# Optimization experiments

Hardware: AMD Instinct MI355X
Metric: run time of the kernel (lower is better)

Reference implementation:

```python
import jax, jax.numpy as jnp
import numpy as np

VOCAB, D_MODEL, N_EXPERTS, TOP_K = 32000, 768, 8, 2
D_FF = 4 * D_MODEL
BATCH, SEQ = 2, 2048


def setup_inputs() -> dict:
    key = jax.random.key(0)
    ks = jax.random.split(key, 6)
    s = 0.02
    return {
        "x": jax.random.randint(ks[0], (BATCH, SEQ), 0, VOCAB),
        "emb": jax.random.normal(ks[1], (VOCAB, D_MODEL), jnp.float32) * s,
        "gate_w": jax.random.normal(ks[2], (D_MODEL, N_EXPERTS), jnp.float32) * s,
        "gate_b": jnp.zeros((N_EXPERTS,), jnp.float32),
        "exp_w": jax.random.normal(ks[3], (N_EXPERTS, D_MODEL, D_FF), jnp.float32) * s,
        "exp_b": jnp.zeros((N_EXPERTS, D_FF), jnp.float32),
        "head_w": jax.random.normal(ks[4], (D_FF, VOCAB), jnp.float32) * s,
        "head_b": jnp.zeros((VOCAB,), jnp.float32),
    }


def reference(x, emb, gate_w, gate_b, exp_w, exp_b, head_w, head_b):
    B, S = x.shape
    h = emb[x]                                   # [B,S,D] embedding gather
    t = h.reshape(B * S, -1)                     # [T,D] token view
    logits = t @ gate_w + gate_b                 # [T,E] router
    topv, topi = jax.lax.top_k(logits, TOP_K)    # top-2 routing
    w = jax.nn.softmax(topv, axis=-1)            # renormalized gate weights
    T = t.shape[0]
    gates = jnp.zeros_like(logits).at[jnp.arange(T)[:, None], topi].set(w)  # [T,E]
    # expert FFN: Linear(d_model -> 4*d_model) + ReLU, dense over experts
    exp_out = jax.nn.relu(jnp.einsum('td,edf->tef', t, exp_w) + exp_b)      # [T,E,F]
    moe = jnp.einsum('te,tef->tf', gates, exp_out)                          # combine
    out = moe @ head_w + head_b                  # [T,V]
    return out.reshape(B, S, -1)
```

## Files before the change

kernel.cpp:

```cpp
#include <hip/hip_runtime.h>

typedef unsigned short u16;
typedef __attribute__((ext_vector_type(8))) short short8;
typedef __attribute__((ext_vector_type(4))) float f32x4;

#define T_TOKENS 4096
#define DMODEL   768
#define DFF      3072
#define NEXP     8
#define NVOCAB   32000

__device__ __forceinline__ u16 f2bf(float f) {
  unsigned u = __float_as_uint(f);
  u += 0x7FFFu + ((u >> 16) & 1u);
  return (u16)(u >> 16);
}

__device__ __forceinline__ void async_load16(const void* g, void* lds) {
  __builtin_amdgcn_global_load_lds((const __attribute__((address_space(1))) void*)g,
                                   (__attribute__((address_space(3))) void*)lds,
                                   16, 0, 0);
}

#define SBAR() __builtin_amdgcn_s_barrier()
#define VMCNT(n) asm volatile("s_waitcnt vmcnt(" #n ")")

__global__ __launch_bounds__(256) void k_embed_router(
    const int* __restrict__ x, const float* __restrict__ emb,
    const float* __restrict__ gw, const float* __restrict__ gb,
    u16* __restrict__ tbf, float* __restrict__ gates)
{
  __shared__ float partial[4][NEXP];
  const int t = blockIdx.x;
  const int tok = x[t];
  const float* er = emb + (size_t)tok * DMODEL;
  float p[NEXP];
#pragma unroll
  for (int e = 0; e < NEXP; ++e) p[e] = 0.f;
#pragma unroll
  for (int i = 0; i < 3; ++i) {
    const int d = threadIdx.x + i * 256;
    const float v = er[d];
    tbf[(size_t)t * DMODEL + d] = f2bf(v);
#pragma unroll
    for (int e = 0; e < NEXP; ++e) p[e] += v * gw[d * NEXP + e];
  }
#pragma unroll
  for (int e = 0; e < NEXP; ++e)
#pragma unroll
    for (int m = 32; m >= 1; m >>= 1) p[e] += __shfl_xor(p[e], m);
  const int lane = threadIdx.x & 63, wv = threadIdx.x >> 6;
  if (lane == 0)
    for (int e = 0; e < NEXP; ++e) partial[wv][e] = p[e];
  __syncthreads();
  if (threadIdx.x == 0) {
    float l[NEXP];
    for (int e = 0; e < NEXP; ++e)
      l[e] = partial[0][e] + partial[1][e] + partial[2][e] + partial[3][e] + gb[e];
    int i0 = 0;
    for (int e = 1; e < NEXP; ++e) if (l[e] > l[i0]) i0 = e;
    int i1 = -1;
    for (int e = 0; e < NEXP; ++e) { if (e == i0) continue; if (i1 < 0 || l[e] > l[i1]) i1 = e; }
    const float w0 = 1.f / (1.f + expf(l[i1] - l[i0]));
    float g[NEXP];
    for (int e = 0; e < NEXP; ++e) g[e] = 0.f;
    g[i0] = w0; g[i1] = 1.f - w0;
    for (int e = 0; e < NEXP; ++e) gates[t * NEXP + e] = g[e];
  }
}

__global__ __launch_bounds__(256) void k_transpose_cvt(
    const float* __restrict__ src, u16* __restrict__ dst, int R, int C)
{
  __shared__ float tile[32][33];
  const float* s = src + (size_t)blockIdx.z * R * C;
  u16* d = dst + (size_t)blockIdx.z * R * C;
  const int tx = threadIdx.x & 31, ty = threadIdx.x >> 5;
  const int c = blockIdx.x * 32 + tx;
#pragma unroll
  for (int i = 0; i < 4; ++i) {
    const int r = blockIdx.y * 32 + ty + i * 8;
    tile[ty + i * 8][tx] = s[(size_t)r * C + c];
  }
  __syncthreads();
  const int rr = blockIdx.y * 32 + tx;
#pragma unroll
  for (int i = 0; i < 4; ++i) {
    const int cc = blockIdx.x * 32 + ty + i * 8;
    d[(size_t)cc * R + rr] = f2bf(tile[tx][ty + i * 8]);
  }
}

__global__ __launch_bounds__(256) void k_ffn(
    const u16* __restrict__ A, const u16* __restrict__ BT,
    const float* __restrict__ gates, const float* __restrict__ eb,
    u16* __restrict__ moe)
{
  __shared__ u16 aT[128 * 64];
  __shared__ u16 bT[128 * 64];
  __shared__ float gLds[128][NEXP];
  const int tid = threadIdx.x;
  const int wave = tid >> 6, lane = tid & 63;
  const int wm = wave >> 1, wn = wave & 1;
  const int kg = lane >> 4, fr = lane & 15;
  const int m0 = blockIdx.y * 128, n0 = blockIdx.x * 128;

  for (int i = tid; i < 128 * NEXP; i += 256)
    gLds[i >> 3][i & 7] = gates[(size_t)(m0 + (i >> 3)) * NEXP + (i & 7)];

  f32x4 macc[4][4] = {};

  for (int e = 0; e < NEXP; ++e) {
    const u16* Be = BT + (size_t)e * DFF * DMODEL;
    f32x4 acc[4][4] = {};
    for (int ks = 0; ks < DMODEL / 64; ++ks) {
      __syncthreads();
      const int kb = ks * 64;
#pragma unroll
      for (int it = 0; it < 4; ++it) {
        const int c = it * 256 + tid;
        const int m = c >> 3;
        const int slot = (c & 7) ^ (m & 7);
        async_load16(A + (size_t)(m0 + m) * DMODEL + kb + slot * 8,
                     &aT[(it * 256 + wave * 64) * 8]);
        async_load16(Be + (size_t)(n0 + m) * DMODEL + kb + slot * 8,
                     &bT[(it * 256 + wave * 64) * 8]);
      }
      __syncthreads();
#pragma unroll
      for (int kk = 0; kk < 2; ++kk) {
        short8 af[4], bf[4];
#pragma unroll
        for (int i = 0; i < 4; ++i) {
          const int am = wm * 64 + i * 16 + fr;
          const int kc = kk * 4 + kg;
          af[i] = *(const short8*)&aT[(am * 8 + (kc ^ (am & 7))) * 8];
          const int bn = wn * 64 + i * 16 + fr;
          bf[i] = *(const short8*)&bT[(bn * 8 + (kc ^ (bn & 7))) * 8];
        }
#pragma unroll
        for (int i = 0; i < 4; ++i)
#pragma unroll
          for (int j = 0; j < 4; ++j)
            acc[i][j] = __builtin_amdgcn_mfma_f32_16x16x32_bf16(af[i], bf[j], acc[i][j], 0, 0, 0);
      }
    }
#pragma unroll
    for (int j = 0; j < 4; ++j) {
      const int col = n0 + wn * 64 + j * 16 + fr;
      const float b = eb[e * DFF + col];
#pragma unroll
      for (int i = 0; i < 4; ++i)
#pragma unroll
        for (int r = 0; r < 4; ++r) {
          float v = acc[i][j][r] + b;
          v = v > 0.f ? v : 0.f;
          macc[i][j][r] += gLds[wm * 64 + i * 16 + kg * 4 + r][e] * v;
        }
    }
  }
#pragma unroll
  for (int i = 0; i < 4; ++i)
#pragma unroll
    for (int r = 0; r < 4; ++r) {
      const int row = m0 + wm * 64 + i * 16 + kg * 4 + r;
#pragma unroll
      for (int j = 0; j < 4; ++j) {
        const int col = n0 + wn * 64 + j * 16 + fr;
        moe[(size_t)row * DFF + col] = f2bf(macc[i][j][r]);
      }
    }
}

__device__ __forceinline__ short8 frag(const u16* buf, int row, int kc) {
  return *(const short8*)(buf + (row * 8 + (kc ^ (row & 7))) * 8);
}

__global__ __launch_bounds__(512, 2) void k_head(
    const u16* __restrict__ A, const u16* __restrict__ BT,
    const float* __restrict__ bias, float* __restrict__ C)
{
  __shared__ u16 aL[2][256 * 64];
  __shared__ u16 bL[2][256 * 64];
  const int tid = threadIdx.x;
  const int lane = tid & 63, wave = tid >> 6;
  const int wm = wave >> 2, wn = wave & 3;
  const int kg = lane >> 4, fr = lane & 15;
  const int wg = (int)blockIdx.x;
  const int swz = (wg & 7) * 250 + (wg >> 3);
  const int m0 = (swz & 15) * 256;
  const int n0 = (swz >> 4) * 256;
  const int K = DFF, NT = K / 64;

  size_t gAo[2], gBo[2]; int lAo[2], lBo[2];
#pragma unroll
  for (int i = 0; i < 2; ++i) {
    const int c = i * 512 + tid, rl = c >> 3, s = c & 7;
    const int rA = (rl & 63) + ((rl >> 6) << 7);
    const int gsA = s ^ (rA & 7);
    gAo[i] = (size_t)(m0 + rA) * K + gsA * 8;
    lAo[i] = rA * 64 + s * 8;
    const int rB = (rl & 31) + ((rl >> 5) << 6);
    const int gsB = s ^ (rB & 7);
    gBo[i] = (size_t)(n0 + rB) * K + gsB * 8;
    lBo[i] = rB * 64 + s * 8;
  }
  auto stageA = [&](int kb, u16* buf, int h) {
#pragma unroll
    for (int i = 0; i < 2; ++i)
      async_load16(A + gAo[i] + (size_t)(h * 64) * K + kb, buf + lAo[i] + h * 4096);
  };
  auto stageB = [&](int kb, u16* buf, int h) {
#pragma unroll
    for (int i = 0; i < 2; ++i)
      async_load16(BT + gBo[i] + (size_t)(h * 32) * K + kb, buf + lBo[i] + h * 2048);
  };

  f32x4 acc[8][4] = {};
  short8 af0[4][2], af1[4][2], bfl[2][2], bfh[2][2];

  stageA(0, aL[0], 0); stageA(0, aL[0], 1);
  stageB(0, bL[0], 0); stageB(0, bL[0], 1);
  stageA(64, aL[1], 0); stageB(64, bL[1], 0); stageA(64, aL[1], 1);
  VMCNT(6);
  __builtin_amdgcn_sched_barrier(0);
  SBAR();
#pragma unroll
  for (int mi = 0; mi < 4; ++mi)
#pragma unroll
    for (int kk = 0; kk < 2; ++kk)
      af0[mi][kk] = frag(aL[0], wm * 128 + mi * 16 + fr, kk * 4 + kg);
#pragma unroll
  for (int ni = 0; ni < 2; ++ni)
#pragma unroll
    for (int kk = 0; kk < 2; ++kk)
      bfl[ni][kk] = frag(bL[0], wn * 64 + ni * 16 + fr, kk * 4 + kg);

  for (int t = 0; t < NT; ++t) {
    const int cur = t & 1;
    const u16* a_ = aL[cur];
    const u16* b_ = bL[cur];
    u16* aw = aL[cur];
    u16* bw = bL[cur];
    const u16* an = aL[cur ^ 1];
    const u16* bn = bL[cur ^ 1];
    const int kb1 = (t + 1) * 64, kb2 = (t + 2) * 64;

#pragma unroll
    for (int ni = 0; ni < 2; ++ni)
#pragma unroll
      for (int kk = 0; kk < 2; ++kk)
        bfh[ni][kk] = frag(b_, wn * 64 + 32 + ni * 16 + fr, kk * 4 + kg);
    if (t + 1 < NT) stageB(kb1, bL[cur ^ 1], 1);
    __builtin_amdgcn_s_setprio(1);
#pragma unroll
    for (int mi = 0; mi < 4; ++mi)
#pragma unroll
      for (int ni = 0; ni < 2; ++ni)
#pragma unroll
        for (int kk = 0; kk < 2; ++kk)
          acc[mi][ni] = __builtin_amdgcn_mfma_f32_16x16x32_bf16(af0[mi][kk], bfl[ni][kk], acc[mi][ni], 0, 0, 0);
    __builtin_amdgcn_s_setprio(0);
    SBAR();

#pragma unroll
    for (int mi = 0; mi < 4; ++mi)
#pragma unroll
      for (int kk = 0; kk < 2; ++kk)
        af1[mi][kk] = frag(a_, wm * 128 + 64 + mi * 16 + fr, kk * 4 + kg);
    if (t + 2 < NT) stageA(kb2, aw, 0);
    __builtin_amdgcn_s_setprio(1);
#pragma unroll
    for (int mi = 0; mi < 4; ++mi)
#pragma unroll
      for (int ni = 0; ni < 2; ++ni)
#pragma unroll
        for (int kk = 0; kk < 2; ++kk)
          acc[mi][ni + 2] = __builtin_amdgcn_mfma_f32_16x16x32_bf16(af0[mi][kk], bfh[ni][kk], acc[mi][ni + 2], 0, 0, 0);
    __builtin_amdgcn_s_setprio(0);
    if (t < NT - 2) { VMCNT(8); } else if (t == NT - 2) { VMCNT(6); }
    __builtin_amdgcn_sched_barrier(0);
    SBAR();

    if (t + 1 < NT) {
#pragma unroll
      for (int mi = 0; mi < 4; ++mi)
#pragma unroll
        for (int kk = 0; kk < 2; ++kk)
          af0[mi][kk] = frag(an, wm * 128 + mi * 16 + fr, kk * 4 + kg);
    }
    if (t + 2 < NT) stageB(kb2, bw, 0);
    __builtin_amdgcn_s_setprio(1);
#pragma unroll
    for (int mi = 0; mi < 4; ++mi)
#pragma unroll
      for (int ni = 0; ni < 2; ++ni)
#pragma unroll
        for (int kk = 0; kk < 2; ++kk)
          acc[mi + 4][ni] = __builtin_amdgcn_mfma_f32_16x16x32_bf16(af1[mi][kk], bfl[ni][kk], acc[mi + 4][ni], 0, 0, 0);
    __builtin_amdgcn_s_setprio(0);
    if (t < NT - 2) { VMCNT(8); } else if (t == NT - 2) { VMCNT(4); }
    __builtin_amdgcn_sched_barrier(0);
    SBAR();

    if (t + 1 < NT) {
#pragma unroll
      for (int ni = 0; ni < 2; ++ni)
#pragma unroll
        for (int kk = 0; kk < 2; ++kk)
          bfl[ni][kk] = frag(bn, wn * 64 + ni * 16 + fr, kk * 4 + kg);
    }
    if (t + 2 < NT) stageA(kb2, aw, 1);
    __builtin_amdgcn_s_setprio(1);
#pragma unroll
    for (int mi = 0; mi < 4; ++mi)
#pragma unroll
      for (int ni = 0; ni < 2; ++ni)
#pragma unroll
        for (int kk = 0; kk < 2; ++kk)
          acc[mi + 4][ni + 2] = __builtin_amdgcn_mfma_f32_16x16x32_bf16(af1[mi][kk], bfh[ni][kk], acc[mi + 4][ni + 2], 0, 0, 0);
    __builtin_amdgcn_s_setprio(0);
    if (t < NT - 2) { VMCNT(6); } else if (t == NT - 2) { VMCNT(0); }
    __builtin_amdgcn_sched_barrier(0);
    SBAR();
  }

#pragma unroll
  for (int ni = 0; ni < 4; ++ni) {
    const int col = n0 + wn * 64 + ni * 16 + fr;
    const float b = bias[col];
#pragma unroll
    for (int mi = 0; mi < 8; ++mi) {
      const int row = m0 + wm * 128 + (mi >> 2) * 64 + (mi & 3) * 16 + kg * 4;
#pragma unroll
      for (int r = 0; r < 4; ++r)
        __builtin_nontemporal_store(acc[mi][ni][r] + b,
                                    &C[(size_t)(row + r) * NVOCAB + col]);
    }
  }
}

extern "C" void kernel_launch(void* const* d_in, const int* in_sizes, int n_in,
                              void* d_out, int out_size, void* d_ws, size_t ws_size,
                              hipStream_t stream) {
  const int*   x     = (const int*)d_in[0];
  const float* emb   = (const float*)d_in[1];
  const float* gw    = (const float*)d_in[2];
  const float* gb    = (const float*)d_in[3];
  const float* expw  = (const float*)d_in[4];
  const float* expb  = (const float*)d_in[5];
  const float* headw = (const float*)d_in[6];
  const float* headb = (const float*)d_in[7];
  float* out = (float*)d_out;

  char* ws = (char*)d_ws;
  size_t off = 0;
  auto alloc = [&](size_t bytes) { size_t r = off; off += (bytes + 255) & ~(size_t)255; return r; };
  u16*   tbf    = (u16*)(ws + alloc((size_t)T_TOKENS * DMODEL * 2));
  float* gates  = (float*)(ws + alloc((size_t)T_TOKENS * NEXP * 4));
  u16*   expwT  = (u16*)(ws + alloc((size_t)NEXP * DFF * DMODEL * 2));
  u16*   headwT = (u16*)(ws + alloc((size_t)NVOCAB * DFF * 2));
  u16*   moe    = (u16*)(ws + alloc((size_t)T_TOKENS * DFF * 2));

  k_embed_router<<<T_TOKENS, 256, 0, stream>>>(x, emb, gw, gb, tbf, gates);
  k_transpose_cvt<<<dim3(DFF / 32, DMODEL / 32, NEXP), 256, 0, stream>>>(expw, expwT, DMODEL, DFF);
  k_transpose_cvt<<<dim3(NVOCAB / 32, DFF / 32, 1), 256, 0, stream>>>(headw, headwT, DFF, NVOCAB);
  k_ffn<<<dim3(DFF / 128, T_TOKENS / 128), 256, 0, stream>>>(tbf, expwT, gates, expb, moe);
  k_head<<<(T_TOKENS / 256) * (NVOCAB / 256), 512, 0, stream>>>(moe, headwT, headb, out);
}
```

Before: 1.389 ms.

## Restructure GEMM main loop into four-phase ping-pong schedule with LDS waits

Reorders the bf16 MFMA main loop so each phase loads its own fragments from the current LDS buffer at the start of the iteration, instead of prefetching next-iteration fragments. Global-to-LDS stage order changes (A half 1 of the next tile staged first), vmcnt waits are removed, and lgkmcnt waits plus extra barriers are added around each phase. The intent is a cleaner ping-pong between LDS reads and MFMA clusters across waves. It adds barriers and drops the explicit vmcnt waits on async loads, which risks stalls or reading LDS before the async loads land.

```diff
diff --git a/kernel.cpp b/kernel.cpp
--- a/kernel.cpp
+++ b/kernel.cpp
@@ -24,6 +24,7 @@
 
 #define SBAR() __builtin_amdgcn_s_barrier()
 #define VMCNT(n) asm volatile("s_waitcnt vmcnt(" #n ")")
+#define LGKM(n)  asm volatile("s_waitcnt lgkmcnt(" #n ")")
 
 __global__ __launch_bounds__(256) void k_embed_router(
     const int* __restrict__ x, const float* __restrict__ emb,
@@ -221,37 +222,32 @@
 
   stageA(0, aL[0], 0); stageA(0, aL[0], 1);
   stageB(0, bL[0], 0); stageB(0, bL[0], 1);
-  stageA(64, aL[1], 0); stageB(64, bL[1], 0); stageA(64, aL[1], 1);
+  stageA(64, aL[1], 0); stageB(64, bL[1], 0); stageB(64, bL[1], 1);
   VMCNT(6);
   __builtin_amdgcn_sched_barrier(0);
   SBAR();
-#pragma unroll
-  for (int mi = 0; mi < 4; ++mi)
-#pragma unroll
-    for (int kk = 0; kk < 2; ++kk)
-      af0[mi][kk] = frag(aL[0], wm * 128 + mi * 16 + fr, kk * 4 + kg);
-#pragma unroll
-  for (int ni = 0; ni < 2; ++ni)
-#pragma unroll
-    for (int kk = 0; kk < 2; ++kk)
-      bfl[ni][kk] = frag(bL[0], wn * 64 + ni * 16 + fr, kk * 4 + kg);
 
   for (int t = 0; t < NT; ++t) {
     const int cur = t & 1;
     const u16* a_ = aL[cur];
     const u16* b_ = bL[cur];
-    u16* aw = aL[cur];
-    u16* bw = bL[cur];
-    const u16* an = aL[cur ^ 1];
-    const u16* bn = bL[cur ^ 1];
     const int kb1 = (t + 1) * 64, kb2 = (t + 2) * 64;
 
 #pragma unroll
+    for (int mi = 0; mi < 4; ++mi)
+#pragma unroll
+      for (int kk = 0; kk < 2; ++kk)
+        af0[mi][kk] = frag(a_, wm * 128 + mi * 16 + fr, kk * 4 + kg);
+#pragma unroll
     for (int ni = 0; ni < 2; ++ni)
 #pragma unroll
       for (int kk = 0; kk < 2; ++kk)
-        bfh[ni][kk] = frag(b_, wn * 64 + 32 + ni * 16 + fr, kk * 4 + kg);
-    if (t + 1 < NT) stageB(kb1, bL[cur ^ 1], 1);
+        bfl[ni][kk] = frag(b_, wn * 64 + ni * 16 + fr, kk * 4 + kg);
+    if (t + 1 < NT) stageA(kb1, aL[cur ^ 1], 1);
+    LGKM(8);
+    SBAR();
+    LGKM(0);
+    __builtin_amdgcn_sched_barrier(0);
     __builtin_amdgcn_s_setprio(1);
 #pragma unroll
     for (int mi = 0; mi < 4; ++mi)
@@ -264,11 +260,14 @@
     SBAR();
 
 #pragma unroll
-    for (int mi = 0; mi < 4; ++mi)
+    for (int ni = 0; ni < 2; ++ni)
 #pragma unroll
       for (int kk = 0; kk < 2; ++kk)
-        af1[mi][kk] = frag(a_, wm * 128 + 64 + mi * 16 + fr, kk * 4 + kg);
-    if (t + 2 < NT) stageA(kb2, aw, 0);
+        bfh[ni][kk] = frag(b_, wn * 64 + 32 + ni * 16 + fr, kk * 4 + kg);
+    if (t + 2 < NT) stageA(kb2, aL[cur], 0);
+    SBAR();
+    LGKM(0);
+    __builtin_amdgcn_sched_barrier(0);
     __builtin_amdgcn_s_setprio(1);
 #pragma unroll
     for (int mi = 0; mi < 4; ++mi)
@@ -278,18 +277,17 @@
         for (int kk = 0; kk < 2; ++kk)
           acc[mi][ni + 2] = __builtin_amdgcn_mfma_f32_16x16x32_bf16(af0[mi][kk], bfh[ni][kk], acc[mi][ni + 2], 0, 0, 0);
     __builtin_amdgcn_s_setprio(0);
-    if (t < NT - 2) { VMCNT(8); } else if (t == NT - 2) { VMCNT(6); }
+    SBAR();
+
+#pragma unroll
+    for (int mi = 0; mi < 4; ++mi)
+#pragma unroll
+      for (int kk = 0; kk < 2; ++kk)
+        af1[mi][kk] = frag(a_, wm * 128 + 64 + mi * 16 + fr, kk * 4 + kg);
+    if (t + 2 < NT) stageB(kb2, bL[cur], 0);
+    SBAR();
+    LGKM(0);
     __builtin_amdgcn_sched_barrier(0);
-    SBAR();
-
-    if (t + 1 < NT) {
-#pragma unroll
-      for (int mi = 0; mi < 4; ++mi)
-#pragma unroll
-        for (int kk = 0; kk < 2; ++kk)
-          af0[mi][kk] = frag(an, wm * 128 + mi * 16 + fr, kk * 4 + kg);
-    }
-    if (t + 2 < NT) stageB(kb2, bw, 0);
     __builtin_amdgcn_s_setprio(1);
 #pragma unroll
     for (int mi = 0; mi < 4; ++mi)
@@ -299,18 +297,10 @@
         for (int kk = 0; kk < 2; ++kk)
           acc[mi + 4][ni] = __builtin_amdgcn_mfma_f32_16x16x32_bf16(af1[mi][kk], bfl[ni][kk], acc[mi + 4][ni], 0, 0, 0);
     __builtin_amdgcn_s_setprio(0);
-    if (t < NT - 2) { VMCNT(8); } else if (t == NT - 2) { VMCNT(4); }
-    __builtin_amdgcn_sched_barrier(0);
-    SBAR();
-
-    if (t + 1 < NT) {
-#pragma unroll
-      for (int ni = 0; ni < 2; ++ni)
-#pragma unroll
-        for (int kk = 0; kk < 2; ++kk)
-          bfl[ni][kk] = frag(bn, wn * 64 + ni * 16 + fr, kk * 4 + kg);
-    }
-    if (t + 2 < NT) stageA(kb2, aw, 1);
+    SBAR();
+
+    if (t + 2 < NT) stageB(kb2, bL[cur], 1);
+    SBAR();
     __builtin_amdgcn_s_setprio(1);
 #pragma unroll
     for (int mi = 0; mi < 4; ++mi)
```

New measurement: 1.493 ms. 1.08x slower.

## Route tokens sparsely to top-2 experts instead of dense all-expert FFN

Applied to the files above, without the earlier changes.

The router now builds per-expert token lists with atomics, split into first- and second-choice slots, instead of a dense gate matrix. The FFN runs as two grouped GEMM launches that gather routed token rows, so each token is computed only for its two experts rather than all eight. The second launch reads the bf16 partial result and adds to it, which adds an extra bf16 rounding step. Atomic list order is nondeterministic, and empty blocks exit early.

```diff
diff --git a/kernel.cpp b/kernel.cpp
--- a/kernel.cpp
+++ b/kernel.cpp
@@ -15,11 +15,13 @@
   u += 0x7FFFu + ((u >> 16) & 1u);
   return (u16)(u >> 16);
 }
+__device__ __forceinline__ float bf2f(u16 b) {
+  return __uint_as_float(((unsigned)b) << 16);
+}
 
 __device__ __forceinline__ void async_load16(const void* g, void* lds) {
   __builtin_amdgcn_global_load_lds((const __attribute__((address_space(1))) void*)g,
-                                   (__attribute__((address_space(3))) void*)lds,
-                                   16, 0, 0);
+                                   (__attribute__((address_space(3))) void*)lds, 16, 0, 0);
 }
 
 #define SBAR() __builtin_amdgcn_s_barrier()
@@ -28,7 +30,8 @@
 __global__ __launch_bounds__(256) void k_embed_router(
     const int* __restrict__ x, const float* __restrict__ emb,
     const float* __restrict__ gw, const float* __restrict__ gb,
-    u16* __restrict__ tbf, float* __restrict__ gates)
+    u16* __restrict__ tbf, int* __restrict__ counts,
+    int* __restrict__ tlist, float* __restrict__ wlist)
 {
   __shared__ float partial[4][NEXP];
   const int t = blockIdx.x;
@@ -62,10 +65,12 @@
     int i1 = -1;
     for (int e = 0; e < NEXP; ++e) { if (e == i0) continue; if (i1 < 0 || l[e] > l[i1]) i1 = e; }
     const float w0 = 1.f / (1.f + expf(l[i1] - l[i0]));
-    float g[NEXP];
-    for (int e = 0; e < NEXP; ++e) g[e] = 0.f;
-    g[i0] = w0; g[i1] = 1.f - w0;
-    for (int e = 0; e < NEXP; ++e) gates[t * NEXP + e] = g[e];
+    int p0 = atomicAdd(&counts[0 * NEXP + i0], 1);
+    tlist[(0 * NEXP + i0) * T_TOKENS + p0] = t;
+    wlist[(0 * NEXP + i0) * T_TOKENS + p0] = w0;
+    int p1 = atomicAdd(&counts[1 * NEXP + i1], 1);
+    tlist[(1 * NEXP + i1) * T_TOKENS + p1] = t;
+    wlist[(1 * NEXP + i1) * T_TOKENS + p1] = 1.f - w0;
   }
 }
 
@@ -91,85 +96,96 @@
   }
 }
 
-__global__ __launch_bounds__(256) void k_ffn(
-    const u16* __restrict__ A, const u16* __restrict__ BT,
-    const float* __restrict__ gates, const float* __restrict__ eb,
+template <int SLOT1>
+__global__ __launch_bounds__(256) void k_ffn_slot(
+    const u16* __restrict__ tbf, const u16* __restrict__ BT,
+    const float* __restrict__ eb, const int* __restrict__ counts,
+    const int* __restrict__ tlist, const float* __restrict__ wlist,
     u16* __restrict__ moe)
 {
+  const int e = blockIdx.z;
+  const int cnt = counts[SLOT1 * NEXP + e];
+  const int mb = blockIdx.y;
+  if (mb * 128 >= cnt) return;
+  const int base = (SLOT1 * NEXP + e) * T_TOKENS + mb * 128;
+  const int lim = cnt - mb * 128;
+
   __shared__ u16 aT[128 * 64];
   __shared__ u16 bT[128 * 64];
-  __shared__ float gLds[128][NEXP];
   const int tid = threadIdx.x;
   const int wave = tid >> 6, lane = tid & 63;
   const int wm = wave >> 1, wn = wave & 1;
   const int kg = lane >> 4, fr = lane & 15;
-  const int m0 = blockIdx.y * 128, n0 = blockIdx.x * 128;
-
-  for (int i = tid; i < 128 * NEXP; i += 256)
-    gLds[i >> 3][i & 7] = gates[(size_t)(m0 + (i >> 3)) * NEXP + (i & 7)];
-
-  f32x4 macc[4][4] = {};
-
-  for (int e = 0; e < NEXP; ++e) {
-    const u16* Be = BT + (size_t)e * DFF * DMODEL;
-    f32x4 acc[4][4] = {};
-    for (int ks = 0; ks < DMODEL / 64; ++ks) {
-      __syncthreads();
-      const int kb = ks * 64;
-#pragma unroll
-      for (int it = 0; it < 4; ++it) {
-        const int c = it * 256 + tid;
-        const int m = c >> 3;
-        const int slot = (c & 7) ^ (m & 7);
-        async_load16(A + (size_t)(m0 + m) * DMODEL + kb + slot * 8,
-                     &aT[(it * 256 + wave * 64) * 8]);
-        async_load16(Be + (size_t)(n0 + m) * DMODEL + kb + slot * 8,
-                     &bT[(it * 256 + wave * 64) * 8]);
+  const int n0 = blockIdx.x * 128;
+  const u16* Be = BT + (size_t)e * DFF * DMODEL;
+
+  int tokm[4];
+#pragma unroll
+  for (int it = 0; it < 4; ++it) {
+    const int m = (it * 256 + tid) >> 3;
+    tokm[it] = tlist[base + (m < lim ? m : lim - 1)];
+  }
+
+  f32x4 acc[4][4] = {};
+  for (int ks = 0; ks < DMODEL / 64; ++ks) {
+    __syncthreads();
+    const int kb = ks * 64;
+#pragma unroll
+    for (int it = 0; it < 4; ++it) {
+      const int c = it * 256 + tid;
+      const int m = c >> 3;
+      const int slot = (c & 7) ^ (m & 7);
+      async_load16(tbf + (size_t)tokm[it] * DMODEL + kb + slot * 8,
+                   &aT[(it * 256 + wave * 64) * 8]);
+      async_load16(Be + (size_t)(n0 + m) * DMODEL + kb + slot * 8,
+                   &bT[(it * 256 + wave * 64) * 8]);
+    }
+    __syncthreads();
+#pragma unroll
+    for (int kk = 0; kk < 2; ++kk) {
+      short8 af[4], bf[4];
+#pragma unroll
+      for (int i = 0; i < 4; ++i) {
+        const int am = wm * 64 + i * 16 + fr;
+        const int kc = kk * 4 + kg;
+        af[i] = *(const short8*)&aT[(am * 8 + (kc ^ (am & 7))) * 8];
+        const int bn = wn * 64 + i * 16 + fr;
+        bf[i] = *(const short8*)&bT[(bn * 8 + (kc ^ (bn & 7))) * 8];
       }
-      __syncthreads();
-#pragma unroll
-      for (int kk = 0; kk < 2; ++kk) {
-        short8 af[4], bf[4];
-#pragma unroll
-        for (int i = 0; i < 4; ++i) {
-          const int am = wm * 64 + i * 16 + fr;
-          const int kc = kk * 4 + kg;
-          af[i] = *(const short8*)&aT[(am * 8 + (kc ^ (am & 7))) * 8];
-          const int bn = wn * 64 + i * 16 + fr;
-          bf[i] = *(const short8*)&bT[(bn * 8 + (kc ^ (bn & 7))) * 8];
-        }
-#pragma unroll
-        for (int i = 0; i < 4; ++i)
-#pragma unroll
-          for (int j = 0; j < 4; ++j)
-            acc[i][j] = __builtin_amdgcn_mfma_f32_16x16x32_bf16(af[i], bf[j], acc[i][j], 0, 0, 0);
+#pragma unroll
+      for (int i = 0; i < 4; ++i)
+#pragma unroll
+        for (int j = 0; j < 4; ++j)
+          acc[i][j] = __builtin_amdgcn_mfma_f32_16x16x32_bf16(af[i], bf[j], acc[i][j], 0, 0, 0);
+    }
+  }
+
+  int trow[4][4]; float wrow[4][4];
+#pragma unroll
+  for (int i = 0; i < 4; ++i)
+#pragma unroll
+    for (int r = 0; r < 4; ++r) {
+      const int row = wm * 64 + i * 16 + kg * 4 + r;
+      if (row < lim) { trow[i][r] = tlist[base + row]; wrow[i][r] = wlist[base + row]; }
+      else trow[i][r] = -1;
+    }
+#pragma unroll
+  for (int j = 0; j < 4; ++j) {
+    const int col = n0 + wn * 64 + j * 16 + fr;
+    const float b = eb[e * DFF + col];
+#pragma unroll
+    for (int i = 0; i < 4; ++i)
+#pragma unroll
+      for (int r = 0; r < 4; ++r) {
+        if (trow[i][r] < 0) continue;
+        float v = acc[i][j][r] + b;
+        v = v > 0.f ? v : 0.f;
+        v *= wrow[i][r];
+        u16* dst = &moe[(size_t)trow[i][r] * DFF + col];
+        if (SLOT1) v += bf2f(*dst);
+        *dst = f2bf(v);
       }
-    }
-#pragma unroll
-    for (int j = 0; j < 4; ++j) {
-      const int col = n0 + wn * 64 + j * 16 + fr;
-      const float b = eb[e * DFF + col];
-#pragma unroll
-      for (int i = 0; i < 4; ++i)
-#pragma unroll
-        for (int r = 0; r < 4; ++r) {
-          float v = acc[i][j][r] + b;
-          v = v > 0.f ? v : 0.f;
-          macc[i][j][r] += gLds[wm * 64 + i * 16 + kg * 4 + r][e] * v;
-        }
-    }
-  }
-#pragma unroll
-  for (int i = 0; i < 4; ++i)
-#pragma unroll
-    for (int r = 0; r < 4; ++r) {
-      const int row = m0 + wm * 64 + i * 16 + kg * 4 + r;
-#pragma unroll
-      for (int j = 0; j < 4; ++j) {
-        const int col = n0 + wn * 64 + j * 16 + fr;
-        moe[(size_t)row * DFF + col] = f2bf(macc[i][j][r]);
-      }
-    }
+  }
 }
 
 __device__ __forceinline__ short8 frag(const u16* buf, int row, int kc) {
@@ -357,14 +373,20 @@
   size_t off = 0;
   auto alloc = [&](size_t bytes) { size_t r = off; off += (bytes + 255) & ~(size_t)255; return r; };
   u16*   tbf    = (u16*)(ws + alloc((size_t)T_TOKENS * DMODEL * 2));
-  float* gates  = (float*)(ws + alloc((size_t)T_TOKENS * NEXP * 4));
+  int*   counts = (int*)(ws + alloc(2 * NEXP * 4));
+  int*   tlist  = (int*)(ws + alloc((size_t)2 * NEXP * T_TOKENS * 4));
+  float* wlist  = (float*)(ws + alloc((size_t)2 * NEXP * T_TOKENS * 4));
   u16*   expwT  = (u16*)(ws + alloc((size_t)NEXP * DFF * DMODEL * 2));
   u16*   headwT = (u16*)(ws + alloc((size_t)NVOCAB * DFF * 2));
   u16*   moe    = (u16*)(ws + alloc((size_t)T_TOKENS * DFF * 2));
 
-  k_embed_router<<<T_TOKENS, 256, 0, stream>>>(x, emb, gw, gb, tbf, gates);
+  hipMemsetAsync(counts, 0, 2 * NEXP * 4, stream);
+  k_embed_router<<<T_TOKENS, 256, 0, stream>>>(x, emb, gw, gb, tbf, counts, tlist, wlist);
   k_transpose_cvt<<<dim3(DFF / 32, DMODEL / 32, NEXP), 256, 0, stream>>>(expw, expwT, DMODEL, DFF);
   k_transpose_cvt<<<dim3(NVOCAB / 32, DFF / 32, 1), 256, 0, stream>>>(headw, headwT, DFF, NVOCAB);
-  k_ffn<<<dim3(DFF / 128, T_TOKENS / 128), 256, 0, stream>>>(tbf, expwT, gates, expb, moe);
+  k_ffn_slot<0><<<dim3(DFF / 128, T_TOKENS / 128, NEXP), 256, 0, stream>>>(
+      tbf, expwT, expb, counts, tlist, wlist, moe);
+  k_ffn_slot<1><<<dim3(DFF / 128, T_TOKENS / 128, NEXP), 256, 0, stream>>>(
+      tbf, expwT, expb, counts, tlist, wlist, moe);
   k_head<<<(T_TOKENS / 256) * (NVOCAB / 256), 512, 0, stream>>>(moe, headwT, headb, out);
 }
```

Measured after the change: 1.246 ms, median of 2. 1.11x faster.
